# Optimization experiments

Hardware: AMD Instinct MI355X
Metric: run time of the kernel (lower is better)

Reference implementation:

```python
import jax, jax.numpy as jnp
import numpy as np
from jax import lax

# Config (matches init_kwargs)
B, CIN, H, W = 32, 256, 56, 56
COUT, KS, STRIDE, PAD, GROUPS = 256, 3, 1, 1, 2
CG_IN = CIN // GROUPS            # 128
OUT_F = COUT // GROUPS           # 128 per-group out features
IN_F = CG_IN * KS * KS           # 1152 per-group in features
Q = (IN_F * OUT_F // 4) * GROUPS # 73728 quadruplets total
TAU = 1.0

# All six 2-of-4 masking patterns (as in the torch module)
_MASK_PATTERNS = np.array([[0.,0.,1.,1.],[0.,1.,0.,1.],[0.,1.,1.,0.],
                           [1.,0.,0.,1.],[1.,0.,1.,0.],[1.,1.,0.,0.]], dtype=np.float32)


def setup_inputs() -> dict:
    key = jax.random.key(0)
    k1, k2, k3, k4 = jax.random.split(key, 4)
    x = jax.random.normal(k1, (B, CIN, H, W), dtype=jnp.float32)
    # per-group weight blocks, xavier-ish scale
    Ws = jax.random.normal(k2, (GROUPS, OUT_F, IN_F), dtype=jnp.float32) * 0.03
    choice_weights = jax.random.normal(k3, (Q, 6), dtype=jnp.float32)
    # gumbel noise: -log(Exp(1)) ~ Gumbel(0,1), matching -empty.exponential_().log()
    gumbels = -jnp.log(jax.random.exponential(k4, (Q, 6), dtype=jnp.float32))
    masking_patterns = jnp.asarray(_MASK_PATTERNS)
    return {"x": x, "Ws": Ws, "choice_weights": choice_weights,
            "gumbels": gumbels, "masking_patterns": masking_patterns}


def _hard_gumbel_softmax(logits, gumbels, tau):
    # straight-through hard gumbel softmax over last dim
    y_soft = jax.nn.softmax((logits + gumbels) / tau, axis=-1)
    idx = jnp.argmax(y_soft, axis=-1)
    y_hard = jax.nn.one_hot(idx, logits.shape[-1], dtype=logits.dtype)
    return y_hard - lax.stop_gradient(y_soft) + y_soft


def reference(x, Ws, choice_weights, gumbels, masking_patterns):
    # 1) sample 2:4 mask per quadruplet via hard gumbel-softmax choice over 6 patterns
    choice = _hard_gumbel_softmax(choice_weights, gumbels, TAU)   # (Q, 6)
    mask = choice @ masking_patterns                              # (Q, 4)
    mask = mask.reshape(GROUPS, OUT_F, IN_F)                      # quadruplets tile W row-major
    Wm = Ws * mask                                                # (G, OUT_F, IN_F)

    # 2) im2col (torch Unfold ordering: channel-major, then kh, kw)
    patches = lax.conv_general_dilated_patches(
        x, filter_shape=(KS, KS), window_strides=(STRIDE, STRIDE),
        padding=[(PAD, PAD), (PAD, PAD)])                         # (B, CIN*KS*KS, Ho, Wo)
    Ho = (H + 2 * PAD - KS) // STRIDE + 1
    Wo = (W + 2 * PAD - KS) // STRIDE + 1
    L = Ho * Wo
    # channel-major ordering => group g occupies contiguous IN_F rows
    patches = patches.reshape(B, GROUPS, IN_F, L)                 # (B, G, IN_F, L)

    # 3) per-group masked GEMM, no bias (use_bias=False)
    y = jnp.einsum('goi,bgil->bgol', Wm, patches)                 # (B, G, OUT_F, L)
    return y.reshape(B, COUT, Ho, Wo)
```

## Files before the change

### kernel.cpp

```cpp
#include <hip/hip_runtime.h>


#define INF   1152
#define HO    56
#define LOUT  3136
#define XP    58

typedef __attribute__((ext_vector_type(8))) short bf16x8;
typedef __attribute__((ext_vector_type(4))) float f32x4;

__device__ __forceinline__ unsigned short f2bf(float f) {
  union { float f; unsigned u; } v; v.f = f;
  unsigned r = v.u + 0x7fffu + ((v.u >> 16) & 1u);
  return (unsigned short)(r >> 16);
}

__device__ __forceinline__ void async_load16(const void* g, void* l) {
  __builtin_amdgcn_global_load_lds(
      (const __attribute__((address_space(1))) void*)g,
      (__attribute__((address_space(3))) void*)l, 16, 0, 0);
}

__global__ __launch_bounds__(256) void prep_kernel(
    const float* __restrict__ x, const float* __restrict__ Ws,
    const float* __restrict__ cw, const float* __restrict__ gb,
    const float* __restrict__ pat,
    unsigned short* __restrict__ Xt, unsigned short* __restrict__ Wt) {
  __shared__ float lds[56 * 129];
  const int t   = threadIdx.x;
  const int bid = blockIdx.x;

  if (bid >= 3712) {
    int idx = (bid - 3712) * 256 + t;
    int c   = idx & 127;
    int of  = (idx >> 7) & 127;
    int gt  = idx >> 14;
    int g   = gt / 9;
    int tap = gt - g * 9;
    int e   = ((g << 7) + of) * INF + c * 9 + tap;
    int q   = e >> 2, pos = e & 3;
    const float* cq = cw + q * 6;
    const float* gq = gb + q * 6;
    float best = cq[0] + gq[0]; int bi = 0;
    #pragma unroll
    for (int j = 1; j < 6; ++j) {
      float v2 = cq[j] + gq[j];
      if (v2 > best) { best = v2; bi = j; }
    }
    Wt[idx] = f2bf(Ws[e] * pat[bi * 4 + pos]);
    return;
  }

  const int bg  = bid / 58;
  const int ihp = bid - bg * 58;
  uint4* dst = (uint4*)(Xt + ((bg * XP + ihp) * XP) * 128);
  if (ihp == 0 || ihp == XP - 1) {
    const uint4 z = {0u, 0u, 0u, 0u};
    for (int i = t; i < XP * 16; i += 256) dst[i] = z;
    return;
  }
  const int ih = ihp - 1;
  const float4* src = (const float4*)(x + (bg * 128) * LOUT + ih * HO);
  for (int i = t; i < 128 * 14; i += 256) {
    int c = i / 14, seg = i - c * 14;
    float4 v = src[c * (LOUT / 4) + seg];
    float* row = &lds[(seg * 4) * 129 + c];
    row[0]       = v.x;
    row[129]     = v.y;
    row[2 * 129] = v.z;
    row[3 * 129] = v.w;
  }
  __syncthreads();
  for (int i = t; i < XP * 16; i += 256) {
    int iwp = i >> 4, oct = i & 15;
    uint4 val = {0u, 0u, 0u, 0u};
    if (iwp != 0 && iwp != XP - 1) {
      const float* s = &lds[(iwp - 1) * 129 + (oct << 3)];
      val.x = (unsigned)f2bf(s[0]) | ((unsigned)f2bf(s[1]) << 16);
      val.y = (unsigned)f2bf(s[2]) | ((unsigned)f2bf(s[3]) << 16);
      val.z = (unsigned)f2bf(s[4]) | ((unsigned)f2bf(s[5]) << 16);
      val.w = (unsigned)f2bf(s[6]) | ((unsigned)f2bf(s[7]) << 16);
    }
    dst[i] = val;
  }
}

__global__ __launch_bounds__(256, 2) void conv_mfma_kernel(
    const unsigned short* __restrict__ Wt, const unsigned short* __restrict__ Xt,
    float* __restrict__ out) {
  __shared__ __align__(16) unsigned short sA[2][128 * 64];
  __shared__ __align__(16) unsigned short sB[2][128 * 64];
  const int t  = threadIdx.x;
  const int ln = t & 63, wv = t >> 6;
  const int wm = wv >> 1, wn = wv & 1;
  const int col = ln & 15, kq = ln >> 4, c7 = col & 7;

  const int lid   = blockIdx.y * 25 + blockIdx.x;
  const int v     = (lid & 7) * 200 + (lid >> 3);
  const int bg    = v / 25;
  const int tileN = v - bg * 25;
  const int g     = bg & 1;
  const int l0    = tileN << 7;

  const int r8 = ln >> 3;
  const int ch = (ln & 7) ^ r8;
  int arow[4], brow[4];
  #pragma unroll
  for (int i = 0; i < 4; ++i) {
    const int rr = (wv << 5) + (i << 3) + r8;
    arow[i] = (rr << 7) + (ch << 3);
    int ll = l0 + rr;
    if (ll > LOUT - 1) ll = LOUT - 1;
    int oh = ll / HO, ow = ll - oh * HO;
    brow[i] = ((bg * XP + oh) * XP + ow) * 128 + (ch << 3);
  }

  f32x4 acc[4][4];
  #pragma unroll
  for (int i = 0; i < 4; ++i)
    #pragma unroll
    for (int j = 0; j < 4; ++j) acc[i][j] = (f32x4){0.f, 0.f, 0.f, 0.f};

  auto issue = [&](int s, int nxt) {
    const int tap = s >> 1, kc = s & 1;
    const int th  = (tap * 11) >> 5;
    const int tw  = tap - th * 3;
    const int bOff = ((th * XP + tw) << 7) + (kc << 6);
    const int aOff = ((g * 9 + tap) << 14) + (kc << 6);
    #pragma unroll
    for (int i = 0; i < 4; ++i) {
      const int lb = ((wv << 5) + (i << 3)) << 6;
      async_load16(Wt + aOff + arow[i], &sA[nxt][lb]);
      async_load16(Xt + bOff + brow[i], &sB[nxt][lb]);
    }
  };

  issue(0, 0);
  __syncthreads();

  #pragma unroll 2
  for (int s = 0; s < 18; ++s) {
    const int cur = s & 1;
    if (s < 17) issue(s + 1, cur ^ 1);
    #pragma unroll
    for (int kh = 0; kh < 2; ++kh) {
      const int pk = (((kh << 2) + kq) ^ c7) << 3;
      bf16x8 af[4], bfr[4];
      #pragma unroll
      for (int mi = 0; mi < 4; ++mi)
        af[mi] = *(const bf16x8*)&sA[cur][(((wm << 6) + (mi << 4) + col) << 6) + pk];
      #pragma unroll
      for (int ni = 0; ni < 4; ++ni)
        bfr[ni] = *(const bf16x8*)&sB[cur][(((wn << 6) + (ni << 4) + col) << 6) + pk];
      #pragma unroll
      for (int mi = 0; mi < 4; ++mi)
        #pragma unroll
        for (int ni = 0; ni < 4; ++ni)
          acc[mi][ni] = __builtin_amdgcn_mfma_f32_16x16x32_bf16(
              af[mi], bfr[ni], acc[mi][ni], 0, 0, 0);
    }
    __syncthreads();
  }

  const int rowq = kq << 2;
  #pragma unroll
  for (int mi = 0; mi < 4; ++mi) {
    #pragma unroll
    for (int ni = 0; ni < 4; ++ni) {
      const int l = l0 + (wn << 6) + (ni << 4) + col;
      if (l < LOUT) {
        #pragma unroll
        for (int r = 0; r < 4; ++r) {
          const int of = (wm << 6) + (mi << 4) + rowq + r;
          out[(bg * 128 + of) * LOUT + l] = acc[mi][ni][r];
        }
      }
    }
  }
}

extern "C" void kernel_launch(void* const* d_in, const int* in_sizes, int n_in,
                              void* d_out, int out_size, void* d_ws, size_t ws_size,
                              hipStream_t stream) {
  const float* x   = (const float*)d_in[0];
  const float* Ws  = (const float*)d_in[1];
  const float* cw  = (const float*)d_in[2];
  const float* gb  = (const float*)d_in[3];
  const float* pat = (const float*)d_in[4];
  float* out = (float*)d_out;

  unsigned short* Wt = (unsigned short*)d_ws;
  unsigned short* Xt = (unsigned short*)((char*)d_ws + (1 << 20));

  prep_kernel<<<4864, 256, 0, stream>>>(x, Ws, cw, gb, pat, Xt, Wt);
  conv_mfma_kernel<<<dim3(25, 64), 256, 0, stream>>>(Wt, Xt, out);
}
```

Baseline: 271.5 us.

## Halve K-tile to 32, raise occupancy, and use explicit waitcnt pipelining

The GEMM K-step shrinks from 64 to 32 channels, halving LDS per block so occupancy can rise from 2 to 4 blocks per CU. The swizzle is recomputed for the narrower rows. The loop now runs 36 steps with manual s_barrier plus vmcnt waits, so the next stage's async loads overlap the current MFMAs, and s_setprio raises priority during the MFMA phase. The cost is twice as many barriers and less compute per synchronisation, plus possible register pressure under the tighter launch bound.

Result: no change. 272.9 us (+0.5%).

```diff
diff --git a/kernel.cpp b/kernel.cpp
--- a/kernel.cpp
+++ b/kernel.cpp
@@ -85,15 +85,15 @@
   }
 }
 
-__global__ __launch_bounds__(256, 2) void conv_mfma_kernel(
+__global__ __launch_bounds__(256, 4) void conv_mfma_kernel(
     const unsigned short* __restrict__ Wt, const unsigned short* __restrict__ Xt,
     float* __restrict__ out) {
-  __shared__ __align__(16) unsigned short sA[2][128 * 64];
-  __shared__ __align__(16) unsigned short sB[2][128 * 64];
+  __shared__ __align__(16) unsigned short sA[2][128 * 32];
+  __shared__ __align__(16) unsigned short sB[2][128 * 32];
   const int t  = threadIdx.x;
   const int ln = t & 63, wv = t >> 6;
   const int wm = wv >> 1, wn = wv & 1;
-  const int col = ln & 15, kq = ln >> 4, c7 = col & 7;
+  const int col = ln & 15, kq = ln >> 4;
 
   const int lid   = blockIdx.y * 25 + blockIdx.x;
   const int v     = (lid & 7) * 200 + (lid >> 3);
@@ -102,64 +102,78 @@
   const int g     = bg & 1;
   const int l0    = tileN << 7;
 
-  const int r8 = ln >> 3;
-  const int ch = (ln & 7) ^ r8;
-  int arow[4], brow[4];
-  #pragma unroll
-  for (int i = 0; i < 4; ++i) {
-    const int rr = (wv << 5) + (i << 3) + r8;
-    arow[i] = (rr << 7) + (ch << 3);
-    int ll = l0 + rr;
+  const int rl = ln >> 2;
+  const int ch = (ln & 3) ^ ((ln >> 3) & 3);
+  int arow[2], brow[2];
+  #pragma unroll
+  for (int i = 0; i < 2; ++i) {
+    const int row = (wv << 5) + (i << 4) + rl;
+    arow[i] = (row << 7) + (ch << 3);
+    int ll = l0 + row;
     if (ll > LOUT - 1) ll = LOUT - 1;
     int oh = ll / HO, ow = ll - oh * HO;
     brow[i] = ((bg * XP + oh) * XP + ow) * 128 + (ch << 3);
   }
 
+  const int slot8 = (kq ^ ((col >> 1) & 3)) << 3;
+  int aoff[4], boff[4];
+  #pragma unroll
+  for (int i = 0; i < 4; ++i) {
+    aoff[i] = (((wm << 6) + (i << 4) + col) << 5) + slot8;
+    boff[i] = (((wn << 6) + (i << 4) + col) << 5) + slot8;
+  }
+
   f32x4 acc[4][4];
   #pragma unroll
   for (int i = 0; i < 4; ++i)
     #pragma unroll
     for (int j = 0; j < 4; ++j) acc[i][j] = (f32x4){0.f, 0.f, 0.f, 0.f};
 
-  auto issue = [&](int s, int nxt) {
-    const int tap = s >> 1, kc = s & 1;
+  auto issue = [&](int s, int b) {
+    const int tap = s >> 2, kc = s & 3;
+    const int c0  = kc << 5;
     const int th  = (tap * 11) >> 5;
     const int tw  = tap - th * 3;
-    const int bOff = ((th * XP + tw) << 7) + (kc << 6);
-    const int aOff = ((g * 9 + tap) << 14) + (kc << 6);
-    #pragma unroll
-    for (int i = 0; i < 4; ++i) {
-      const int lb = ((wv << 5) + (i << 3)) << 6;
-      async_load16(Wt + aOff + arow[i], &sA[nxt][lb]);
-      async_load16(Xt + bOff + brow[i], &sB[nxt][lb]);
+    const int aT  = ((g * 9 + tap) << 14) + c0;
+    const int bT  = ((th * XP + tw) << 7) + c0;
+    #pragma unroll
+    for (int i = 0; i < 2; ++i) {
+      const int lb = (wv << 10) + (i << 9);
+      async_load16(Wt + aT + arow[i], &sA[b][lb]);
+      async_load16(Xt + bT + brow[i], &sB[b][lb]);
     }
   };
 
   issue(0, 0);
-  __syncthreads();
-
-  #pragma unroll 2
-  for (int s = 0; s < 18; ++s) {
+
+  #pragma unroll 1
+  for (int s = 0; s < 36; ++s) {
     const int cur = s & 1;
-    if (s < 17) issue(s + 1, cur ^ 1);
-    #pragma unroll
-    for (int kh = 0; kh < 2; ++kh) {
-      const int pk = (((kh << 2) + kq) ^ c7) << 3;
-      bf16x8 af[4], bfr[4];
-      #pragma unroll
-      for (int mi = 0; mi < 4; ++mi)
-        af[mi] = *(const bf16x8*)&sA[cur][(((wm << 6) + (mi << 4) + col) << 6) + pk];
+    __builtin_amdgcn_s_barrier();
+    if (s < 35) {
+      issue(s + 1, cur ^ 1);
+      asm volatile("s_waitcnt vmcnt(4)" ::: "memory");
+    } else {
+      asm volatile("s_waitcnt vmcnt(0)" ::: "memory");
+    }
+    __builtin_amdgcn_sched_barrier(0);
+    __builtin_amdgcn_s_barrier();
+
+    __builtin_amdgcn_s_setprio(1);
+    bf16x8 af[4], bfr[4];
+    #pragma unroll
+    for (int mi = 0; mi < 4; ++mi)
+      af[mi] = *(const bf16x8*)&sA[cur][aoff[mi]];
+    #pragma unroll
+    for (int ni = 0; ni < 4; ++ni)
+      bfr[ni] = *(const bf16x8*)&sB[cur][boff[ni]];
+    #pragma unroll
+    for (int mi = 0; mi < 4; ++mi)
       #pragma unroll
       for (int ni = 0; ni < 4; ++ni)
-        bfr[ni] = *(const bf16x8*)&sB[cur][(((wn << 6) + (ni << 4) + col) << 6) + pk];
-      #pragma unroll
-      for (int mi = 0; mi < 4; ++mi)
-        #pragma unroll
-        for (int ni = 0; ni < 4; ++ni)
-          acc[mi][ni] = __builtin_amdgcn_mfma_f32_16x16x32_bf16(
-              af[mi], bfr[ni], acc[mi][ni], 0, 0, 0);
-    }
-    __syncthreads();
+        acc[mi][ni] = __builtin_amdgcn_mfma_f32_16x16x32_bf16(
+            af[mi], bfr[ni], acc[mi][ni], 0, 0, 0);
+    __builtin_amdgcn_s_setprio(0);
   }
 
   const int rowq = kq << 2;
```
